# Kernel optimization log

Hardware: AMD Instinct MI355X
Metric: run time of the kernel (lower is better)

The kernel has to match this reference:

```python
import jax, jax.numpy as jnp
import numpy as np

B, N, T, D = 4, 170, 96, 256
H, HD = 8, 32          # num_heads, head_dim
TD, HIST, P = 24, 3, 16  # traffic_dim, history_size, num_patterns


def setup_inputs() -> dict:
    key = jax.random.key(0)
    ks = jax.random.split(key, 15)
    s = 0.02
    return {
        "query": jax.random.normal(ks[0], (B, N, T, D), jnp.float32),
        "key": jax.random.normal(ks[1], (B, N, T, D), jnp.float32),
        "value": jax.random.normal(ks[2], (B, N, T, D), jnp.float32),
        "pattern_matrix": jax.random.normal(ks[3], (P, HIST, TD), jnp.float32),
        "Wp": jax.random.normal(ks[4], (TD, TD), jnp.float32) * s,
        "bp": jnp.zeros((TD,), jnp.float32),
        "Wq": jax.random.normal(ks[5], (D, D), jnp.float32) * s,
        "bq": jnp.zeros((D,), jnp.float32),
        "Wk": jax.random.normal(ks[6], (D, D), jnp.float32) * s,
        "bk": jnp.zeros((D,), jnp.float32),
        "Wv": jax.random.normal(ks[7], (D, D), jnp.float32) * s,
        "bv": jnp.zeros((D,), jnp.float32),
        "Wo": jax.random.normal(ks[8], (D, D), jnp.float32) * s,
        "bo": jnp.zeros((D,), jnp.float32),
    }


def _forward(query, key, value, pattern_matrix, Wp, bp, Wq, bq, Wk, bk, Wv, bv, Wo, bo):
    b, n, t, d = query.shape
    # ---- compute_similarity: sliding windows over the traffic features ----
    tf = query[..., :TD]  # [B,N,T,TD]
    L = t - HIST + 1
    # windows[b,n,l,j,c] = tf[b,n,l+j,c]  (same as F.unfold with kernel (HIST,1))
    windows = jnp.stack([tf[:, :, j:j + L, :] for j in range(HIST)], axis=3)  # [B,N,L,HIST,TD]
    history_pattern = pattern_matrix @ Wp.T + bp  # [P,HIST,TD]
    # einsum('bhd,phd->bph') then mean over h == einsum over d, sum over h / HIST
    sim = jnp.einsum('bnlhd,phd->bnlp', windows, history_pattern) / HIST  # [B,N,L,P]
    pad = (HIST - 1) // 2
    sim = jnp.pad(sim, ((0, 0), (0, 0), (pad, pad), (0, 0)))  # [B,N,T,P]

    # ---- generate_temporal_mask ----
    sim_mean = sim.mean(axis=1)  # [B,T,P]
    temporal_weights = jax.nn.softmax(sim_mean, axis=-1).sum(axis=-1, keepdims=True)  # [B,T,1]
    tmask = temporal_weights @ jnp.swapaxes(temporal_weights, 1, 2)  # [B,T,T]
    # expand to [B,H,N,T,T] then flatten (torch indexing: b*H+h)
    mask_flat = jnp.broadcast_to(tmask[:, None, None, :, :], (b, H, n, t, t)).reshape(b * H, n, t, t)

    # ---- projections + head split (torch split/cat -> head-major batch: h*B+b) ----
    q = query @ Wq.T + bq
    k = key @ Wk.T + bk
    v = value @ Wv.T + bv
    def split_heads(x):
        return x.reshape(b, n, t, H, HD).transpose(3, 0, 1, 2, 4).reshape(H * b, n, t, HD)
    q, k, v = split_heads(q), split_heads(k), split_heads(v)

    scores = jnp.einsum('anqd,ankd->anqk', q, k) / jnp.sqrt(jnp.float32(HD))  # [H*B,N,T,T]
    scores = scores * mask_flat  # elementwise (shapes match; torch mixes head/batch order the same way)
    attn = jax.nn.softmax(scores, axis=-1)  # dropout is identity in eval mode
    out = jnp.einsum('anqk,ankd->anqd', attn, v)  # [H*B,N,T,HD]
    out = out.reshape(H, b, n, t, HD).transpose(1, 2, 3, 0, 4).reshape(b, n, t, d)
    return out @ Wo.T + bo


def reference(query, key, value, pattern_matrix, Wp, bp, Wq, bq, Wk, bk, Wv, bv, Wo, bo):
    return _forward(query, key, value, pattern_matrix, Wp, bp, Wq, bq, Wk, bk, Wv, bv, Wo, bo)
```

## Files before the change

### kernel.cpp

```cpp
#include <hip/hip_runtime.h>
#include <math.h>

#define B_  4
#define N_  170
#define T_  96
#define D_  256
#define H_  8
#define HD_ 32
#define BN_ (B_*N_)
#define WSZ (D_*D_)

typedef short  bf16x8 __attribute__((ext_vector_type(8)));
typedef float  f32x4  __attribute__((ext_vector_type(4)));

#define XB   0
#define KB   49152
#define VB   98304
#define LDSZ 147456

__device__ __forceinline__ ushort to_bf16(float x)
{
    uint u = __builtin_bit_cast(uint, x);
    u += 0x8000u;
    return (ushort)(u >> 16);
}

__device__ __forceinline__ uint pack2(float x0, float x1)
{
    return (uint)to_bf16(x0) | ((uint)to_bf16(x1) << 16);
}

__device__ __forceinline__ uint4 pack8(float4 a0, float4 a1)
{
    uint4 r;
    r.x = pack2(a0.x, a0.y); r.y = pack2(a0.z, a0.w);
    r.z = pack2(a1.x, a1.y); r.w = pack2(a1.z, a1.w);
    return r;
}

#define MFMA(a, b, c) __builtin_amdgcn_mfma_f32_16x16x32_bf16((a), (b), (c), 0, 0, 0)

__global__ __launch_bounds__(256)
void splitw_kernel(const float* __restrict__ Wq, const float* __restrict__ Wk,
                   const float* __restrict__ Wv, const float* __restrict__ Wo,
                   ushort* __restrict__ whi)
{
    const int gid = blockIdx.x * 256 + threadIdx.x;
    const int mat = gid >> 13;
    const int rem = gid & 8191;
    const int col = rem >> 5;
    const int kc  = rem & 31;
    const float* W = (mat == 0) ? Wq : (mat == 1) ? Wk : (mat == 2) ? Wv : Wo;
    const float s  = (mat == 0) ? 0.17677669529663687f : 1.0f;
    const float* p = W + (size_t)col * D_ + kc * 8;
    float4 a0 = *(const float4*)p;
    float4 a1 = *(const float4*)(p + 4);
    a0.x *= s; a0.y *= s; a0.z *= s; a0.w *= s;
    a1.x *= s; a1.y *= s; a1.z *= s; a1.w *= s;
    const size_t off = (size_t)mat * WSZ + ((size_t)kc * 256 + col) * 8;
    *(uint4*)(whi + off) = pack8(a0, a1);
}

__global__ __launch_bounds__(1024)
void mega_kernel(const float* __restrict__ Xq, const float* __restrict__ Xk,
                 const float* __restrict__ Xv, const ushort* __restrict__ W,
                 const float* __restrict__ bq, const float* __restrict__ bk,
                 const float* __restrict__ bv, const float* __restrict__ bo,
                 float* __restrict__ out)
{
    __shared__ __align__(16) char lds[LDSZ];

    const int bn   = blockIdx.x;
    const int tid  = threadIdx.x;
    const int wv   = tid >> 6;
    const int lane = tid & 63;
    const int lr   = lane & 15;
    const int kgl  = lane >> 4;
    const int h    = wv >> 1;
    const int ib   = (wv & 1) * 3;
    const size_t xoff = (size_t)bn * T_ * D_;

    int srow[3], skc[3]; uint saddr[3];
    #pragma unroll
    for (int c = 0; c < 3; c++) {
        const int cc = tid + c * 1024;
        const int row = cc % 96, kc = cc / 96;
        srow[c] = row; skc[c] = kc;
        saddr[c] = (uint)(((((kc >> 2) * 6 + (row >> 4)) * 4 + (kc & 3)) * 256)
                          + (row & 15) * 16);
    }

    #pragma unroll
    for (int c = 0; c < 3; c++) {
        const float* p = Xq + xoff + srow[c] * D_ + skc[c] * 8;
        float4 a0 = *(const float4*)p, a1 = *(const float4*)(p + 4);
        *(uint4*)(lds + XB + saddr[c]) = pack8(a0, a1);
    }
    float4 pf[6];
    #pragma unroll
    for (int c = 0; c < 3; c++) {
        const float* p = Xk + xoff + srow[c] * D_ + skc[c] * 8;
        pf[2*c] = *(const float4*)p; pf[2*c+1] = *(const float4*)(p + 4);
    }
    __syncthreads();

    #pragma unroll
    for (int c = 0; c < 3; c++)
        *(uint4*)(lds + KB + saddr[c]) = pack8(pf[2*c], pf[2*c+1]);
    #pragma unroll
    for (int c = 0; c < 3; c++) {
        const float* p = Xv + xoff + srow[c] * D_ + skc[c] * 8;
        pf[2*c] = *(const float4*)p; pf[2*c+1] = *(const float4*)(p + 4);
    }
    {
        bf16x8 wf[8];
        #pragma unroll
        for (int ks = 0; ks < 8; ks++)
            wf[ks] = *(const bf16x8*)(W + ((size_t)(ks*4+kgl)*256 + wv*16 + lr)*8);
        f32x4 acc[6];
        #pragma unroll
        for (int nt = 0; nt < 6; nt++) acc[nt] = (f32x4)0.f;
        #pragma unroll
        for (int ks = 0; ks < 8; ks++)
            #pragma unroll
            for (int nt = 0; nt < 6; nt++) {
                bf16x8 xb = *(const bf16x8*)(lds + XB + ((ks*6+nt)*4+kgl)*256 + lr*16);
                acc[nt] = MFMA(wf[ks], xb, acc[nt]);
            }
        const float qs = 0.17677669529663687f;
        const int kg = (wv & 1)*2 + (kgl >> 1);
        float4 b4 = *(const float4*)(bq + wv*16 + kgl*4);
        #pragma unroll
        for (int nt = 0; nt < 6; nt++) {
            ushort4 o;
            o.x = to_bf16(acc[nt][0] + b4.x*qs);
            o.y = to_bf16(acc[nt][1] + b4.y*qs);
            o.z = to_bf16(acc[nt][2] + b4.z*qs);
            o.w = to_bf16(acc[nt][3] + b4.w*qs);
            *(ushort4*)(lds + VB + ((h*6+nt)*4+kg)*256 + lr*16 + (kgl&1)*8) = o;
        }
    }
    __syncthreads();

    #pragma unroll
    for (int c = 0; c < 3; c++)
        *(uint4*)(lds + XB + saddr[c]) = pack8(pf[2*c], pf[2*c+1]);
    bf16x8 qf[3];
    #pragma unroll
    for (int j = 0; j < 3; j++)
        qf[j] = *(const bf16x8*)(lds + VB + ((h*6 + ib + j)*4 + kgl)*256 + lr*16);
    f32x4 kacc[6];
    {
        const ushort* Wk = W + WSZ;
        bf16x8 wf[8];
        #pragma unroll
        for (int ks = 0; ks < 8; ks++)
            wf[ks] = *(const bf16x8*)(Wk + ((size_t)(ks*4+kgl)*256 + wv*16 + lr)*8);
        #pragma unroll
        for (int nt = 0; nt < 6; nt++) kacc[nt] = (f32x4)0.f;
        #pragma unroll
        for (int ks = 0; ks < 8; ks++)
            #pragma unroll
            for (int nt = 0; nt < 6; nt++) {
                bf16x8 xb = *(const bf16x8*)(lds + KB + ((ks*6+nt)*4+kgl)*256 + lr*16);
                kacc[nt] = MFMA(wf[ks], xb, kacc[nt]);
            }
    }
    __syncthreads();

    {
        const int kg = (wv & 1)*2 + (kgl >> 1);
        float4 b4 = *(const float4*)(bk + wv*16 + kgl*4);
        #pragma unroll
        for (int nt = 0; nt < 6; nt++) {
            ushort4 o;
            o.x = to_bf16(kacc[nt][0] + b4.x);
            o.y = to_bf16(kacc[nt][1] + b4.y);
            o.z = to_bf16(kacc[nt][2] + b4.z);
            o.w = to_bf16(kacc[nt][3] + b4.w);
            *(ushort4*)(lds + KB + ((h*6+nt)*4+kg)*256 + lr*16 + (kgl&1)*8) = o;
        }
    }
    {
        const ushort* Wv = W + 2*WSZ;
        bf16x8 wf[8];
        #pragma unroll
        for (int ks = 0; ks < 8; ks++)
            wf[ks] = *(const bf16x8*)(Wv + ((size_t)(ks*4+kgl)*256 + wv*16 + lr)*8);
        f32x4 av[6];
        #pragma unroll
        for (int mt = 0; mt < 6; mt++) av[mt] = (f32x4)0.f;
        #pragma unroll
        for (int ks = 0; ks < 8; ks++)
            #pragma unroll
            for (int mt = 0; mt < 6; mt++) {
                bf16x8 xa = *(const bf16x8*)(lds + XB + ((ks*6+mt)*4+kgl)*256 + lr*16);
                av[mt] = MFMA(xa, wf[ks], av[mt]);
            }
        const int n2v = wv & 1;
        const float bvv = bv[wv*16 + lr];
        #pragma unroll
        for (int mt = 0; mt < 6; mt++) {
            const int kvkg = mt*2 + (kgl >> 1);
            const int s2 = kvkg >> 2, kgv = kvkg & 3;
            ushort4 o;
            o.x = to_bf16(av[mt][0] + bvv);
            o.y = to_bf16(av[mt][1] + bvv);
            o.z = to_bf16(av[mt][2] + bvv);
            o.w = to_bf16(av[mt][3] + bvv);
            *(ushort4*)(lds + VB + (((h*3+s2)*2+n2v)*4+kgv)*256 + lr*16 + (kgl&1)*8) = o;
        }
    }
    __syncthreads();

    f32x4 oacc[3][2];
    #pragma unroll
    for (int j = 0; j < 3; j++) { oacc[j][0] = (f32x4)0.f; oacc[j][1] = (f32x4)0.f; }
    {
        char* sw = lds + XB + wv * 3072;
        #pragma unroll
        for (int j = 0; j < 3; j++) {
            f32x4 s[6];
            #pragma unroll
            for (int mt = 0; mt < 6; mt++) {
                bf16x8 kf = *(const bf16x8*)(lds + KB + ((h*6+mt)*4+kgl)*256 + lr*16);
                s[mt] = MFMA(kf, qf[j], (f32x4)0.f);
            }
            float mx = s[0][0];
            #pragma unroll
            for (int mt = 0; mt < 6; mt++)
                #pragma unroll
                for (int r = 0; r < 4; r++) mx = fmaxf(mx, s[mt][r]);
            mx = fmaxf(mx, __shfl_xor(mx, 16));
            mx = fmaxf(mx, __shfl_xor(mx, 32));
            float sum = 0.f;
            #pragma unroll
            for (int mt = 0; mt < 6; mt++)
                #pragma unroll
                for (int r = 0; r < 4; r++) {
                    float e = __expf(s[mt][r] - mx);
                    s[mt][r] = e; sum += e;
                }
            sum += __shfl_xor(sum, 16);
            sum += __shfl_xor(sum, 32);
            const float inv = 1.f / sum;
            #pragma unroll
            for (int mt = 0; mt < 6; mt++) {
                uint2 u2;
                u2.x = pack2(s[mt][0]*inv, s[mt][1]*inv);
                u2.y = pack2(s[mt][2]*inv, s[mt][3]*inv);
                *(uint2*)(sw + (mt*2 + (kgl>>1))*256 + lr*16 + (kgl&1)*8) = u2;
            }
            #pragma unroll
            for (int s2 = 0; s2 < 3; s2++) {
                bf16x8 pa = *(const bf16x8*)(sw + (s2*4+kgl)*256 + lr*16);
                #pragma unroll
                for (int n2 = 0; n2 < 2; n2++) {
                    bf16x8 vf = *(const bf16x8*)(lds + VB + (((h*3+s2)*2+n2)*4+kgl)*256 + lr*16);
                    oacc[j][n2] = MFMA(pa, vf, oacc[j][n2]);
                }
            }
        }
    }
    __syncthreads();

    #pragma unroll
    for (int j = 0; j < 3; j++)
        #pragma unroll
        for (int n2 = 0; n2 < 2; n2++) {
            const int dcol = h*32 + n2*16 + lr;
            const int kc   = dcol >> 3;
            const int irow = ib + j;
            char* base = lds + XB + (((kc>>2)*6 + irow)*4 + (kc&3))*256 + (dcol&7)*2;
            #pragma unroll
            for (int r = 0; r < 4; r++)
                *(ushort*)(base + (kgl*4+r)*16) = to_bf16(oacc[j][n2][r]);
        }
    __syncthreads();

    {
        const ushort* Wo = W + 3*WSZ;
        bf16x8 wf[8];
        #pragma unroll
        for (int ks = 0; ks < 8; ks++)
            wf[ks] = *(const bf16x8*)(Wo + ((size_t)(ks*4+kgl)*256 + wv*16 + lr)*8);
        f32x4 a2[6];
        #pragma unroll
        for (int mt = 0; mt < 6; mt++) a2[mt] = (f32x4)0.f;
        #pragma unroll
        for (int ks = 0; ks < 8; ks++)
            #pragma unroll
            for (int mt = 0; mt < 6; mt++) {
                bf16x8 oa = *(const bf16x8*)(lds + XB + ((ks*6+mt)*4+kgl)*256 + lr*16);
                a2[mt] = MFMA(oa, wf[ks], a2[mt]);
            }
        const float bod = bo[wv*16 + lr];
        #pragma unroll
        for (int mt = 0; mt < 6; mt++)
            #pragma unroll
            for (int r = 0; r < 4; r++) {
                const int t = mt*16 + kgl*4 + r;
                out[((size_t)(bn*T_ + t))*D_ + wv*16 + lr] = a2[mt][r] + bod;
            }
    }
}

extern "C" void kernel_launch(void* const* d_in, const int* in_sizes, int n_in,
                              void* d_out, int out_size, void* d_ws, size_t ws_size,
                              hipStream_t stream)
{
    const float* query = (const float*)d_in[0];
    const float* key   = (const float*)d_in[1];
    const float* value = (const float*)d_in[2];
    const float* Wq = (const float*)d_in[6];
    const float* bq = (const float*)d_in[7];
    const float* Wk = (const float*)d_in[8];
    const float* bk = (const float*)d_in[9];
    const float* Wv = (const float*)d_in[10];
    const float* bv = (const float*)d_in[11];
    const float* Wo = (const float*)d_in[12];
    const float* bo = (const float*)d_in[13];

    float*  out = (float*)d_out;
    ushort* whi = (ushort*)d_ws;

    splitw_kernel<<<dim3(128), 256, 0, stream>>>(Wq, Wk, Wv, Wo, whi);
    mega_kernel<<<dim3(BN_), 1024, 0, stream>>>(
        query, key, value, whi, bq, bk, bv, bo, out);
}
```

Baseline: 102.2 us.

## Switch projection GEMMs to 32x32x16 MFMA with uneven wave work split

Rewrites the four 256x256 projection GEMMs (Q, K, V, O) to use 32x32x16 bf16 MFMA tiles instead of 16x16x32, with new fragment addressing macros and epilogues. Each of the 16 waves owns a 32-column output slice. Waves 0-7 compute two 32-row time tiles and waves 8-15 compute one, which covers the 96 rows. The larger MFMA tile is meant to cut LDS fragment loads and instruction count per FLOP. In exchange, half the waves do double work, leaving the load unbalanced across the block.

```diff
diff --git a/kernel.cpp b/kernel.cpp
--- a/kernel.cpp
+++ b/kernel.cpp
@@ -12,6 +12,7 @@
 
 typedef short  bf16x8 __attribute__((ext_vector_type(8)));
 typedef float  f32x4  __attribute__((ext_vector_type(4)));
+typedef float  f32x16 __attribute__((ext_vector_type(16)));
 
 #define XB   0
 #define KB   49152
@@ -38,7 +39,8 @@
     return r;
 }
 
-#define MFMA(a, b, c) __builtin_amdgcn_mfma_f32_16x16x32_bf16((a), (b), (c), 0, 0, 0)
+#define MFMA16(a, b, c) __builtin_amdgcn_mfma_f32_16x16x32_bf16((a), (b), (c), 0, 0, 0)
+#define MFMA32(a, b, c) __builtin_amdgcn_mfma_f32_32x32x16_bf16((a), (b), (c), 0, 0, 0)
 
 __global__ __launch_bounds__(256)
 void splitw_kernel(const float* __restrict__ Wq, const float* __restrict__ Wk,
@@ -76,8 +78,14 @@
     const int lane = tid & 63;
     const int lr   = lane & 15;
     const int kgl  = lane >> 4;
+    const int l31  = lane & 31;
+    const int l5   = lane >> 5;
+    const int l4   = kgl & 1;
     const int h    = wv >> 1;
     const int ib   = (wv & 1) * 3;
+    const bool heavy = (wv < 8);
+    const int dt   = wv & 7;
+    const int tt0  = heavy ? 0 : 1;
     const size_t xoff = (size_t)bn * T_ * D_;
 
     int srow[3], skc[3]; uint saddr[3];
@@ -90,6 +98,37 @@
                           + (row & 15) * 16);
     }
 
+#define XFRAG(base, tt_, ks_) \
+    (*(const bf16x8*)(lds + (base) + \
+        ((((ks_) >> 1) * 24 + ((tt_) * 2 + l4) * 4 + (((ks_) & 1) * 2 + l5)) * 256) \
+        + lr * 16))
+#define WFRAG(mat, ks_) \
+    (*(const bf16x8*)((mat) + ((size_t)((ks_) * 2 + l5) * 256 + dt * 32 + l31) * 8))
+#define QK_EPI(ACC, tt_, bp, sc, RB) do { \
+        _Pragma("unroll") \
+        for (int g = 0; g < 4; g++) { \
+            float4 b4 = *(const float4*)((bp) + dt*32 + 8*g + 4*l5); \
+            ushort4 o; \
+            o.x = to_bf16(ACC[4*g+0] + b4.x*(sc)); \
+            o.y = to_bf16(ACC[4*g+1] + b4.y*(sc)); \
+            o.z = to_bf16(ACC[4*g+2] + b4.z*(sc)); \
+            o.w = to_bf16(ACC[4*g+3] + b4.w*(sc)); \
+            *(ushort4*)(lds + (RB) + ((dt*6 + 2*(tt_) + l4)*4 + g)*256 + lr*16 + l5*8) = o; \
+        } \
+    } while (0)
+#define V_EPI(ACC, tt_) do { \
+        const float bvv_ = bv[dt*32 + l31]; \
+        _Pragma("unroll") \
+        for (int g = 0; g < 4; g++) { \
+            ushort4 o; \
+            o.x = to_bf16(ACC[4*g+0] + bvv_); \
+            o.y = to_bf16(ACC[4*g+1] + bvv_); \
+            o.z = to_bf16(ACC[4*g+2] + bvv_); \
+            o.w = to_bf16(ACC[4*g+3] + bvv_); \
+            *(ushort4*)(lds + VB + (((dt*3 + (tt_))*2 + l4)*4 + g)*256 + lr*16 + l5*8) = o; \
+        } \
+    } while (0)
+
     #pragma unroll
     for (int c = 0; c < 3; c++) {
         const float* p = Xq + xoff + srow[c] * D_ + skc[c] * 8;
@@ -113,32 +152,16 @@
         pf[2*c] = *(const float4*)p; pf[2*c+1] = *(const float4*)(p + 4);
     }
     {
-        bf16x8 wf[8];
-        #pragma unroll
-        for (int ks = 0; ks < 8; ks++)
-            wf[ks] = *(const bf16x8*)(W + ((size_t)(ks*4+kgl)*256 + wv*16 + lr)*8);
-        f32x4 acc[6];
-        #pragma unroll
-        for (int nt = 0; nt < 6; nt++) acc[nt] = (f32x4)0.f;
-        #pragma unroll
-        for (int ks = 0; ks < 8; ks++)
-            #pragma unroll
-            for (int nt = 0; nt < 6; nt++) {
-                bf16x8 xb = *(const bf16x8*)(lds + XB + ((ks*6+nt)*4+kgl)*256 + lr*16);
-                acc[nt] = MFMA(wf[ks], xb, acc[nt]);
-            }
+        f32x16 a0 = (f32x16)0.f, a1 = (f32x16)0.f;
+        #pragma unroll
+        for (int ks = 0; ks < 16; ks++) {
+            bf16x8 wf = WFRAG(W, ks);
+            a0 = MFMA32(wf, XFRAG(XB, tt0, ks), a0);
+            if (heavy) a1 = MFMA32(wf, XFRAG(XB, 2, ks), a1);
+        }
         const float qs = 0.17677669529663687f;
-        const int kg = (wv & 1)*2 + (kgl >> 1);
-        float4 b4 = *(const float4*)(bq + wv*16 + kgl*4);
-        #pragma unroll
-        for (int nt = 0; nt < 6; nt++) {
-            ushort4 o;
-            o.x = to_bf16(acc[nt][0] + b4.x*qs);
-            o.y = to_bf16(acc[nt][1] + b4.y*qs);
-            o.z = to_bf16(acc[nt][2] + b4.z*qs);
-            o.w = to_bf16(acc[nt][3] + b4.w*qs);
-            *(ushort4*)(lds + VB + ((h*6+nt)*4+kg)*256 + lr*16 + (kgl&1)*8) = o;
-        }
+        QK_EPI(a0, tt0, bq, qs, VB);
+        if (heavy) QK_EPI(a1, 2, bq, qs, VB);
     }
     __syncthreads();
 
@@ -149,67 +172,31 @@
     #pragma unroll
     for (int j = 0; j < 3; j++)
         qf[j] = *(const bf16x8*)(lds + VB + ((h*6 + ib + j)*4 + kgl)*256 + lr*16);
-    f32x4 kacc[6];
+    f32x16 k0 = (f32x16)0.f, k1 = (f32x16)0.f;
     {
         const ushort* Wk = W + WSZ;
-        bf16x8 wf[8];
-        #pragma unroll
-        for (int ks = 0; ks < 8; ks++)
-            wf[ks] = *(const bf16x8*)(Wk + ((size_t)(ks*4+kgl)*256 + wv*16 + lr)*8);
-        #pragma unroll
-        for (int nt = 0; nt < 6; nt++) kacc[nt] = (f32x4)0.f;
-        #pragma unroll
-        for (int ks = 0; ks < 8; ks++)
-            #pragma unroll
-            for (int nt = 0; nt < 6; nt++) {
-                bf16x8 xb = *(const bf16x8*)(lds + KB + ((ks*6+nt)*4+kgl)*256 + lr*16);
-                kacc[nt] = MFMA(wf[ks], xb, kacc[nt]);
-            }
-    }
-    __syncthreads();
-
-    {
-        const int kg = (wv & 1)*2 + (kgl >> 1);
-        float4 b4 = *(const float4*)(bk + wv*16 + kgl*4);
-        #pragma unroll
-        for (int nt = 0; nt < 6; nt++) {
-            ushort4 o;
-            o.x = to_bf16(kacc[nt][0] + b4.x);
-            o.y = to_bf16(kacc[nt][1] + b4.y);
-            o.z = to_bf16(kacc[nt][2] + b4.z);
-            o.w = to_bf16(kacc[nt][3] + b4.w);
-            *(ushort4*)(lds + KB + ((h*6+nt)*4+kg)*256 + lr*16 + (kgl&1)*8) = o;
-        }
-    }
+        #pragma unroll
+        for (int ks = 0; ks < 16; ks++) {
+            bf16x8 wf = WFRAG(Wk, ks);
+            k0 = MFMA32(wf, XFRAG(KB, tt0, ks), k0);
+            if (heavy) k1 = MFMA32(wf, XFRAG(KB, 2, ks), k1);
+        }
+    }
+    __syncthreads();
+
+    QK_EPI(k0, tt0, bk, 1.0f, KB);
+    if (heavy) QK_EPI(k1, 2, bk, 1.0f, KB);
     {
         const ushort* Wv = W + 2*WSZ;
-        bf16x8 wf[8];
-        #pragma unroll
-        for (int ks = 0; ks < 8; ks++)
-            wf[ks] = *(const bf16x8*)(Wv + ((size_t)(ks*4+kgl)*256 + wv*16 + lr)*8);
-        f32x4 av[6];
-        #pragma unroll
-        for (int mt = 0; mt < 6; mt++) av[mt] = (f32x4)0.f;
-        #pragma unroll
-        for (int ks = 0; ks < 8; ks++)
-            #pragma unroll
-            for (int mt = 0; mt < 6; mt++) {
-                bf16x8 xa = *(const bf16x8*)(lds + XB + ((ks*6+mt)*4+kgl)*256 + lr*16);
-                av[mt] = MFMA(xa, wf[ks], av[mt]);
-            }
-        const int n2v = wv & 1;
-        const float bvv = bv[wv*16 + lr];
-        #pragma unroll
-        for (int mt = 0; mt < 6; mt++) {
-            const int kvkg = mt*2 + (kgl >> 1);
-            const int s2 = kvkg >> 2, kgv = kvkg & 3;
-            ushort4 o;
-            o.x = to_bf16(av[mt][0] + bvv);
-            o.y = to_bf16(av[mt][1] + bvv);
-            o.z = to_bf16(av[mt][2] + bvv);
-            o.w = to_bf16(av[mt][3] + bvv);
-            *(ushort4*)(lds + VB + (((h*3+s2)*2+n2v)*4+kgv)*256 + lr*16 + (kgl&1)*8) = o;
-        }
+        f32x16 a0 = (f32x16)0.f, a1 = (f32x16)0.f;
+        #pragma unroll
+        for (int ks = 0; ks < 16; ks++) {
+            bf16x8 wf = WFRAG(Wv, ks);
+            a0 = MFMA32(XFRAG(XB, tt0, ks), wf, a0);
+            if (heavy) a1 = MFMA32(XFRAG(XB, 2, ks), wf, a1);
+        }
+        V_EPI(a0, tt0);
+        if (heavy) V_EPI(a1, 2);
     }
     __syncthreads();
 
@@ -224,7 +211,7 @@
             #pragma unroll
             for (int mt = 0; mt < 6; mt++) {
                 bf16x8 kf = *(const bf16x8*)(lds + KB + ((h*6+mt)*4+kgl)*256 + lr*16);
-                s[mt] = MFMA(kf, qf[j], (f32x4)0.f);
+                s[mt] = MFMA16(kf, qf[j], (f32x4)0.f);
             }
             float mx = s[0][0];
             #pragma unroll
@@ -257,7 +244,7 @@
                 #pragma unroll
                 for (int n2 = 0; n2 < 2; n2++) {
                     bf16x8 vf = *(const bf16x8*)(lds + VB + (((h*3+s2)*2+n2)*4+kgl)*256 + lr*16);
-                    oacc[j][n2] = MFMA(pa, vf, oacc[j][n2]);
+                    oacc[j][n2] = MFMA16(pa, vf, oacc[j][n2]);
                 }
             }
         }
@@ -280,29 +267,35 @@
 
     {
         const ushort* Wo = W + 3*WSZ;
-        bf16x8 wf[8];
-        #pragma unroll
-        for (int ks = 0; ks < 8; ks++)
-            wf[ks] = *(const bf16x8*)(Wo + ((size_t)(ks*4+kgl)*256 + wv*16 + lr)*8);
-        f32x4 a2[6];
-        #pragma unroll
-        for (int mt = 0; mt < 6; mt++) a2[mt] = (f32x4)0.f;
-        #pragma unroll
-        for (int ks = 0; ks < 8; ks++)
-            #pragma unroll
-            for (int mt = 0; mt < 6; mt++) {
-                bf16x8 oa = *(const bf16x8*)(lds + XB + ((ks*6+mt)*4+kgl)*256 + lr*16);
-                a2[mt] = MFMA(oa, wf[ks], a2[mt]);
+        f32x16 a0 = (f32x16)0.f, a1 = (f32x16)0.f;
+        #pragma unroll
+        for (int ks = 0; ks < 16; ks++) {
+            bf16x8 wf = WFRAG(Wo, ks);
+            a0 = MFMA32(XFRAG(XB, tt0, ks), wf, a0);
+            if (heavy) a1 = MFMA32(XFRAG(XB, 2, ks), wf, a1);
+        }
+        const float bod = bo[dt*32 + l31];
+        #pragma unroll
+        for (int g = 0; g < 4; g++)
+            #pragma unroll
+            for (int r = 0; r < 4; r++) {
+                const int t = tt0*32 + 8*g + 4*l5 + r;
+                out[((size_t)(bn*T_ + t))*D_ + dt*32 + l31] = a0[4*g+r] + bod;
             }
-        const float bod = bo[wv*16 + lr];
-        #pragma unroll
-        for (int mt = 0; mt < 6; mt++)
-            #pragma unroll
-            for (int r = 0; r < 4; r++) {
-                const int t = mt*16 + kgl*4 + r;
-                out[((size_t)(bn*T_ + t))*D_ + wv*16 + lr] = a2[mt][r] + bod;
-            }
-    }
+        if (heavy) {
+            #pragma unroll
+            for (int g = 0; g < 4; g++)
+                #pragma unroll
+                for (int r = 0; r < 4; r++) {
+                    const int t = 2*32 + 8*g + 4*l5 + r;
+                    out[((size_t)(bn*T_ + t))*D_ + dt*32 + l31] = a1[4*g+r] + bod;
+                }
+        }
+    }
+#undef XFRAG
+#undef WFRAG
+#undef QK_EPI
+#undef V_EPI
 }
 
 extern "C" void kernel_launch(void* const* d_in, const int* in_sizes, int n_in,
```

Measured after the change: 133.9 us. 1.31x slower.

## Split attention kernel by head halves and move output projection to separate GEMM

Applied to the files above, without the earlier changes.

The fused kernel now runs two 512-thread blocks per (b,n), each handling four heads and half the projection columns. The K dimension of each QKV projection is streamed in two halves to shrink LDS use, which should let more blocks stay resident per CU. The output projection moves to a separate tiled GEMM kernel that reads a bf16 intermediate buffer and double-buffers its tiles with async global-to-LDS loads. In exchange, the intermediate attention output makes an extra round trip through global memory, there are more barriers, and each input X tile is now read by both blocks that share a (b,n).

```diff
diff --git a/kernel.cpp b/kernel.cpp
--- a/kernel.cpp
+++ b/kernel.cpp
@@ -7,16 +7,18 @@
 #define D_  256
 #define H_  8
 #define HD_ 32
+#define R_  (B_*N_*T_)
 #define BN_ (B_*N_)
 #define WSZ (D_*D_)
 
 typedef short  bf16x8 __attribute__((ext_vector_type(8)));
 typedef float  f32x4  __attribute__((ext_vector_type(4)));
+typedef unsigned int u32;
 
 #define XB   0
-#define KB   49152
-#define VB   98304
-#define LDSZ 147456
+#define KB   24576
+#define VB   49152
+#define LDSZ 73728
 
 __device__ __forceinline__ ushort to_bf16(float x)
 {
@@ -39,6 +41,14 @@
 }
 
 #define MFMA(a, b, c) __builtin_amdgcn_mfma_f32_16x16x32_bf16((a), (b), (c), 0, 0, 0)
+
+__device__ __forceinline__ void async_load16(const void* g, void* l)
+{
+    __builtin_amdgcn_global_load_lds(
+        (const u32 __attribute__((address_space(1)))*)g,
+        (u32 __attribute__((address_space(3)))*)l,
+        16, 0, 0);
+}
 
 __global__ __launch_bounds__(256)
 void splitw_kernel(const float* __restrict__ Wq, const float* __restrict__ Wk,
@@ -61,116 +71,125 @@
     *(uint4*)(whi + off) = pack8(a0, a1);
 }
 
-__global__ __launch_bounds__(1024)
+__global__ __launch_bounds__(512)
 void mega_kernel(const float* __restrict__ Xq, const float* __restrict__ Xk,
                  const float* __restrict__ Xv, const ushort* __restrict__ W,
                  const float* __restrict__ bq, const float* __restrict__ bk,
-                 const float* __restrict__ bv, const float* __restrict__ bo,
-                 float* __restrict__ out)
+                 const float* __restrict__ bv, ushort* __restrict__ obuf)
 {
     __shared__ __align__(16) char lds[LDSZ];
 
-    const int bn   = blockIdx.x;
+    const int bx   = blockIdx.x;
+    const int bn   = bx >> 1;
+    const int hb   = bx & 1;
     const int tid  = threadIdx.x;
     const int wv   = tid >> 6;
     const int lane = tid & 63;
     const int lr   = lane & 15;
     const int kgl  = lane >> 4;
-    const int h    = wv >> 1;
+    const int hl   = wv >> 1;
     const int ib   = (wv & 1) * 3;
+    const int dc0  = hb * 128;
     const size_t xoff = (size_t)bn * T_ * D_;
 
     int srow[3], skc[3]; uint saddr[3];
     #pragma unroll
     for (int c = 0; c < 3; c++) {
-        const int cc = tid + c * 1024;
+        const int cc = tid + c * 512;
         const int row = cc % 96, kc = cc / 96;
         srow[c] = row; skc[c] = kc;
         saddr[c] = (uint)(((((kc >> 2) * 6 + (row >> 4)) * 4 + (kc & 3)) * 256)
                           + (row & 15) * 16);
     }
 
-    #pragma unroll
-    for (int c = 0; c < 3; c++) {
-        const float* p = Xq + xoff + srow[c] * D_ + skc[c] * 8;
-        float4 a0 = *(const float4*)p, a1 = *(const float4*)(p + 4);
-        *(uint4*)(lds + XB + saddr[c]) = pack8(a0, a1);
-    }
     float4 pf[6];
-    #pragma unroll
-    for (int c = 0; c < 3; c++) {
-        const float* p = Xk + xoff + srow[c] * D_ + skc[c] * 8;
-        pf[2*c] = *(const float4*)p; pf[2*c+1] = *(const float4*)(p + 4);
-    }
-    __syncthreads();
-
-    #pragma unroll
-    for (int c = 0; c < 3; c++)
-        *(uint4*)(lds + KB + saddr[c]) = pack8(pf[2*c], pf[2*c+1]);
-    #pragma unroll
-    for (int c = 0; c < 3; c++) {
-        const float* p = Xv + xoff + srow[c] * D_ + skc[c] * 8;
-        pf[2*c] = *(const float4*)p; pf[2*c+1] = *(const float4*)(p + 4);
-    }
+#define PFETCH(X, kh) do { \
+        _Pragma("unroll") \
+        for (int c = 0; c < 3; c++) { \
+            const float* p_ = (X) + xoff + srow[c] * D_ + (kh) * 128 + skc[c] * 8; \
+            pf[2*c] = *(const float4*)p_; pf[2*c+1] = *(const float4*)(p_ + 4); \
+        } \
+    } while (0)
+#define STW() do { \
+        _Pragma("unroll") \
+        for (int c = 0; c < 3; c++) \
+            *(uint4*)(lds + XB + saddr[c]) = pack8(pf[2*c], pf[2*c+1]); \
+    } while (0)
+#define GEMM_WN(Wbase, kh, ACC) do { \
+        _Pragma("unroll") \
+        for (int ksl = 0; ksl < 4; ksl++) { \
+            bf16x8 wf = *(const bf16x8*)((Wbase) + \
+                ((size_t)((kh)*16 + ksl*4 + kgl)*256 + dc0 + wv*16 + lr)*8); \
+            _Pragma("unroll") \
+            for (int nt = 0; nt < 6; nt++) { \
+                bf16x8 xb = *(const bf16x8*)(lds + XB + ((ksl*6+nt)*4+kgl)*256 + lr*16); \
+                ACC[nt] = MFMA(wf, xb, ACC[nt]); \
+            } \
+        } \
+    } while (0)
+#define GEMM_NW(Wbase, kh, ACC) do { \
+        _Pragma("unroll") \
+        for (int ksl = 0; ksl < 4; ksl++) { \
+            bf16x8 wf = *(const bf16x8*)((Wbase) + \
+                ((size_t)((kh)*16 + ksl*4 + kgl)*256 + dc0 + wv*16 + lr)*8); \
+            _Pragma("unroll") \
+            for (int mt = 0; mt < 6; mt++) { \
+                bf16x8 xa = *(const bf16x8*)(lds + XB + ((ksl*6+mt)*4+kgl)*256 + lr*16); \
+                ACC[mt] = MFMA(xa, wf, ACC[mt]); \
+            } \
+        } \
+    } while (0)
+
+    PFETCH(Xq, 0); STW();
+    PFETCH(Xq, 1);
+    __syncthreads();
+
+    f32x4 qacc[6];
+    #pragma unroll
+    for (int nt = 0; nt < 6; nt++) qacc[nt] = (f32x4)0.f;
+    GEMM_WN(W, 0, qacc);
+    __syncthreads();
+
+    STW(); PFETCH(Xk, 0);
+    __syncthreads();
+
+    GEMM_WN(W, 1, qacc);
     {
-        bf16x8 wf[8];
-        #pragma unroll
-        for (int ks = 0; ks < 8; ks++)
-            wf[ks] = *(const bf16x8*)(W + ((size_t)(ks*4+kgl)*256 + wv*16 + lr)*8);
-        f32x4 acc[6];
-        #pragma unroll
-        for (int nt = 0; nt < 6; nt++) acc[nt] = (f32x4)0.f;
-        #pragma unroll
-        for (int ks = 0; ks < 8; ks++)
-            #pragma unroll
-            for (int nt = 0; nt < 6; nt++) {
-                bf16x8 xb = *(const bf16x8*)(lds + XB + ((ks*6+nt)*4+kgl)*256 + lr*16);
-                acc[nt] = MFMA(wf[ks], xb, acc[nt]);
-            }
         const float qs = 0.17677669529663687f;
         const int kg = (wv & 1)*2 + (kgl >> 1);
-        float4 b4 = *(const float4*)(bq + wv*16 + kgl*4);
+        float4 b4 = *(const float4*)(bq + dc0 + wv*16 + kgl*4);
         #pragma unroll
         for (int nt = 0; nt < 6; nt++) {
             ushort4 o;
-            o.x = to_bf16(acc[nt][0] + b4.x*qs);
-            o.y = to_bf16(acc[nt][1] + b4.y*qs);
-            o.z = to_bf16(acc[nt][2] + b4.z*qs);
-            o.w = to_bf16(acc[nt][3] + b4.w*qs);
-            *(ushort4*)(lds + VB + ((h*6+nt)*4+kg)*256 + lr*16 + (kgl&1)*8) = o;
-        }
-    }
-    __syncthreads();
-
-    #pragma unroll
-    for (int c = 0; c < 3; c++)
-        *(uint4*)(lds + XB + saddr[c]) = pack8(pf[2*c], pf[2*c+1]);
+            o.x = to_bf16(qacc[nt][0] + b4.x*qs);
+            o.y = to_bf16(qacc[nt][1] + b4.y*qs);
+            o.z = to_bf16(qacc[nt][2] + b4.z*qs);
+            o.w = to_bf16(qacc[nt][3] + b4.w*qs);
+            *(ushort4*)(lds + VB + ((hl*6+nt)*4+kg)*256 + lr*16 + (kgl&1)*8) = o;
+        }
+    }
+    __syncthreads();
+
+    STW(); PFETCH(Xk, 1);
+    __syncthreads();
+
+    f32x4 kacc[6];
+    #pragma unroll
+    for (int nt = 0; nt < 6; nt++) kacc[nt] = (f32x4)0.f;
+    GEMM_WN(W + WSZ, 0, kacc);
     bf16x8 qf[3];
     #pragma unroll
     for (int j = 0; j < 3; j++)
-        qf[j] = *(const bf16x8*)(lds + VB + ((h*6 + ib + j)*4 + kgl)*256 + lr*16);
-    f32x4 kacc[6];
-    {
-        const ushort* Wk = W + WSZ;
-        bf16x8 wf[8];
-        #pragma unroll
-        for (int ks = 0; ks < 8; ks++)
-            wf[ks] = *(const bf16x8*)(Wk + ((size_t)(ks*4+kgl)*256 + wv*16 + lr)*8);
-        #pragma unroll
-        for (int nt = 0; nt < 6; nt++) kacc[nt] = (f32x4)0.f;
-        #pragma unroll
-        for (int ks = 0; ks < 8; ks++)
-            #pragma unroll
-            for (int nt = 0; nt < 6; nt++) {
-                bf16x8 xb = *(const bf16x8*)(lds + KB + ((ks*6+nt)*4+kgl)*256 + lr*16);
-                kacc[nt] = MFMA(wf[ks], xb, kacc[nt]);
-            }
-    }
-    __syncthreads();
-
+        qf[j] = *(const bf16x8*)(lds + VB + ((hl*6 + ib + j)*4 + kgl)*256 + lr*16);
+    __syncthreads();
+
+    STW(); PFETCH(Xv, 0);
+    __syncthreads();
+
+    GEMM_WN(W + WSZ, 1, kacc);
     {
         const int kg = (wv & 1)*2 + (kgl >> 1);
-        float4 b4 = *(const float4*)(bk + wv*16 + kgl*4);
+        float4 b4 = *(const float4*)(bk + dc0 + wv*16 + kgl*4);
         #pragma unroll
         for (int nt = 0; nt < 6; nt++) {
             ushort4 o;
@@ -178,37 +197,37 @@
             o.y = to_bf16(kacc[nt][1] + b4.y);
             o.z = to_bf16(kacc[nt][2] + b4.z);
             o.w = to_bf16(kacc[nt][3] + b4.w);
-            *(ushort4*)(lds + KB + ((h*6+nt)*4+kg)*256 + lr*16 + (kgl&1)*8) = o;
-        }
-    }
+            *(ushort4*)(lds + KB + ((hl*6+nt)*4+kg)*256 + lr*16 + (kgl&1)*8) = o;
+        }
+    }
+    __syncthreads();
+
+    STW(); PFETCH(Xv, 1);
+    __syncthreads();
+
+    f32x4 vacc[6];
+    #pragma unroll
+    for (int mt = 0; mt < 6; mt++) vacc[mt] = (f32x4)0.f;
+    GEMM_NW(W + 2*WSZ, 0, vacc);
+    __syncthreads();
+
+    STW();
+    __syncthreads();
+
+    GEMM_NW(W + 2*WSZ, 1, vacc);
     {
-        const ushort* Wv = W + 2*WSZ;
-        bf16x8 wf[8];
-        #pragma unroll
-        for (int ks = 0; ks < 8; ks++)
-            wf[ks] = *(const bf16x8*)(Wv + ((size_t)(ks*4+kgl)*256 + wv*16 + lr)*8);
-        f32x4 av[6];
-        #pragma unroll
-        for (int mt = 0; mt < 6; mt++) av[mt] = (f32x4)0.f;
-        #pragma unroll
-        for (int ks = 0; ks < 8; ks++)
-            #pragma unroll
-            for (int mt = 0; mt < 6; mt++) {
-                bf16x8 xa = *(const bf16x8*)(lds + XB + ((ks*6+mt)*4+kgl)*256 + lr*16);
-                av[mt] = MFMA(xa, wf[ks], av[mt]);
-            }
         const int n2v = wv & 1;
-        const float bvv = bv[wv*16 + lr];
+        const float bvv = bv[dc0 + wv*16 + lr];
         #pragma unroll
         for (int mt = 0; mt < 6; mt++) {
             const int kvkg = mt*2 + (kgl >> 1);
             const int s2 = kvkg >> 2, kgv = kvkg & 3;
             ushort4 o;
-            o.x = to_bf16(av[mt][0] + bvv);
-            o.y = to_bf16(av[mt][1] + bvv);
-            o.z = to_bf16(av[mt][2] + bvv);
-            o.w = to_bf16(av[mt][3] + bvv);
-            *(ushort4*)(lds + VB + (((h*3+s2)*2+n2v)*4+kgv)*256 + lr*16 + (kgl&1)*8) = o;
+            o.x = to_bf16(vacc[mt][0] + bvv);
+            o.y = to_bf16(vacc[mt][1] + bvv);
+            o.z = to_bf16(vacc[mt][2] + bvv);
+            o.w = to_bf16(vacc[mt][3] + bvv);
+            *(ushort4*)(lds + VB + (((hl*3+s2)*2+n2v)*4+kgv)*256 + lr*16 + (kgl&1)*8) = o;
         }
     }
     __syncthreads();
@@ -223,7 +242,7 @@
             f32x4 s[6];
             #pragma unroll
             for (int mt = 0; mt < 6; mt++) {
-                bf16x8 kf = *(const bf16x8*)(lds + KB + ((h*6+mt)*4+kgl)*256 + lr*16);
+                bf16x8 kf = *(const bf16x8*)(lds + KB + ((hl*6+mt)*4+kgl)*256 + lr*16);
                 s[mt] = MFMA(kf, qf[j], (f32x4)0.f);
             }
             float mx = s[0][0];
@@ -256,52 +275,114 @@
                 bf16x8 pa = *(const bf16x8*)(sw + (s2*4+kgl)*256 + lr*16);
                 #pragma unroll
                 for (int n2 = 0; n2 < 2; n2++) {
-                    bf16x8 vf = *(const bf16x8*)(lds + VB + (((h*3+s2)*2+n2)*4+kgl)*256 + lr*16);
+                    bf16x8 vf = *(const bf16x8*)(lds + VB + (((hl*3+s2)*2+n2)*4+kgl)*256 + lr*16);
                     oacc[j][n2] = MFMA(pa, vf, oacc[j][n2]);
                 }
             }
         }
     }
-    __syncthreads();
 
     #pragma unroll
     for (int j = 0; j < 3; j++)
         #pragma unroll
         for (int n2 = 0; n2 < 2; n2++) {
-            const int dcol = h*32 + n2*16 + lr;
-            const int kc   = dcol >> 3;
-            const int irow = ib + j;
-            char* base = lds + XB + (((kc>>2)*6 + irow)*4 + (kc&3))*256 + (dcol&7)*2;
-            #pragma unroll
-            for (int r = 0; r < 4; r++)
-                *(ushort*)(base + (kgl*4+r)*16) = to_bf16(oacc[j][n2][r]);
-        }
-    __syncthreads();
-
-    {
-        const ushort* Wo = W + 3*WSZ;
-        bf16x8 wf[8];
-        #pragma unroll
-        for (int ks = 0; ks < 8; ks++)
-            wf[ks] = *(const bf16x8*)(Wo + ((size_t)(ks*4+kgl)*256 + wv*16 + lr)*8);
-        f32x4 a2[6];
-        #pragma unroll
-        for (int mt = 0; mt < 6; mt++) a2[mt] = (f32x4)0.f;
-        #pragma unroll
-        for (int ks = 0; ks < 8; ks++)
-            #pragma unroll
-            for (int mt = 0; mt < 6; mt++) {
-                bf16x8 oa = *(const bf16x8*)(lds + XB + ((ks*6+mt)*4+kgl)*256 + lr*16);
-                a2[mt] = MFMA(oa, wf[ks], a2[mt]);
+            const int col = dc0 + hl*32 + n2*16 + lr;
+            #pragma unroll
+            for (int r = 0; r < 4; r++) {
+                const int t = (ib + j)*16 + kgl*4 + r;
+                obuf[((size_t)(bn*T_ + t))*D_ + col] = to_bf16(oacc[j][n2][r]);
             }
-        const float bod = bo[wv*16 + lr];
-        #pragma unroll
-        for (int mt = 0; mt < 6; mt++)
-            #pragma unroll
-            for (int r = 0; r < 4; r++) {
-                const int t = mt*16 + kgl*4 + r;
-                out[((size_t)(bn*T_ + t))*D_ + wv*16 + lr] = a2[mt][r] + bod;
+        }
+#undef PFETCH
+#undef STW
+#undef GEMM_WN
+#undef GEMM_NW
+}
+
+__global__ __launch_bounds__(256)
+void wo_kernel(const ushort* __restrict__ Obf, const ushort* __restrict__ whi,
+               const float* __restrict__ bo, float* __restrict__ io)
+{
+    const int tid  = threadIdx.x;
+    const int lane = tid & 63;
+    const int w    = tid >> 6;
+    const int col0 = blockIdx.x * 128;
+    const int row0 = blockIdx.y * 128;
+    const int wr   = w >> 1;
+    const int wc   = w & 1;
+    const int lr   = lane & 15;
+    const int kgl  = lane >> 4;
+    const ushort* Wh = whi + (size_t)3 * WSZ;
+
+    __shared__ __align__(16) char Alds[2][8320];
+    __shared__ __align__(16) char Blds[2][8320];
+
+    const ushort* pa[2];
+    uint wa[2];
+    #pragma unroll
+    for (int i = 0; i < 2; i++) {
+        const int s = w * 2 + i, kg = s >> 1, rhalf = s & 1;
+        pa[i] = Obf + (size_t)(row0 + rhalf * 64 + lane) * D_ + kg * 8;
+        wa[i] = (uint)__builtin_amdgcn_readfirstlane((kg * 130 + rhalf * 64) * 16);
+    }
+    const ushort* pb[2];
+    uint wb[2];
+    #pragma unroll
+    for (int i = 0; i < 2; i++) {
+        const int s = w * 2 + i, kg = s >> 1, colh = s & 1;
+        pb[i] = Wh + ((size_t)kg * 256 + col0 + colh * 64 + lane) * 8;
+        wb[i] = (uint)__builtin_amdgcn_readfirstlane((kg * 130 + colh * 64) * 16);
+    }
+
+    f32x4 acc[4][4];
+    #pragma unroll
+    for (int m = 0; m < 4; m++)
+        #pragma unroll
+        for (int n = 0; n < 4; n++) acc[m][n] = (f32x4)0.f;
+
+    #pragma unroll
+    for (int i = 0; i < 2; i++) async_load16(pa[i], Alds[0] + wa[i]);
+    #pragma unroll
+    for (int i = 0; i < 2; i++) async_load16(pb[i], Blds[0] + wb[i]);
+    __syncthreads();
+
+    for (int t = 0; t < 8; t++) {
+        const int cur = t & 1, nxt = cur ^ 1;
+        if (t < 7) {
+            #pragma unroll
+            for (int i = 0; i < 2; i++)
+                async_load16(pa[i] + (size_t)(t + 1) * 32, Alds[nxt] + wa[i]);
+            #pragma unroll
+            for (int i = 0; i < 2; i++)
+                async_load16(pb[i] + (size_t)(t + 1) * 8192, Blds[nxt] + wb[i]);
+        }
+        bf16x8 a[4];
+        #pragma unroll
+        for (int m = 0; m < 4; m++)
+            a[m] = *(const bf16x8*)(Alds[cur] + (kgl*130 + wr*64 + m*16 + lr) * 16);
+        #pragma unroll
+        for (int n = 0; n < 4; n++) {
+            const int cb = wc*64 + n*16 + lr;
+            bf16x8 bh = *(const bf16x8*)(Blds[cur] + (kgl*130 + cb) * 16);
+            #pragma unroll
+            for (int m = 0; m < 4; m++)
+                acc[m][n] = MFMA(a[m], bh, acc[m][n]);
+        }
+        __syncthreads();
+    }
+
+    #pragma unroll
+    for (int n = 0; n < 4; n++) {
+        const int gcol = col0 + wc*64 + n*16 + lr;
+        const float bv = bo[gcol];
+        #pragma unroll
+        for (int m = 0; m < 4; m++) {
+            #pragma unroll
+            for (int reg = 0; reg < 4; reg++) {
+                const int grow = row0 + wr*64 + m*16 + kgl*4 + reg;
+                io[(size_t)grow * D_ + gcol] = acc[m][n][reg] + bv;
             }
+        }
     }
 }
 
@@ -321,10 +402,12 @@
     const float* Wo = (const float*)d_in[12];
     const float* bo = (const float*)d_in[13];
 
-    float*  out = (float*)d_out;
-    ushort* whi = (ushort*)d_ws;
+    float*  out  = (float*)d_out;
+    ushort* whi  = (ushort*)d_ws;
+    ushort* obuf = whi + (size_t)4 * WSZ;
 
     splitw_kernel<<<dim3(128), 256, 0, stream>>>(Wq, Wk, Wv, Wo, whi);
-    mega_kernel<<<dim3(BN_), 1024, 0, stream>>>(
-        query, key, value, whi, bq, bk, bv, bo, out);
-}
+    mega_kernel<<<dim3(BN_ * 2), 512, 0, stream>>>(
+        query, key, value, whi, bq, bk, bv, obuf);
+    wo_kernel<<<dim3(2, R_ / 128), 256, 0, stream>>>(obuf, whi, bo, out);
+}
```

New measurement: 180.2 us. 1.76x slower.
